# Performance work log

Measured on AMD Instinct MI355X. Metric: run time of the kernel, lower is better.

The kernel has to match this reference:

```python
import jax, jax.numpy as jnp
import numpy as np

B, S, D = 4, 2048, 1024
H = 16
HD = D // H  # 64


def setup_inputs() -> dict:
    key = jax.random.key(0)
    ks = jax.random.split(key, 6)
    s = 0.02
    return {
        "x": jax.random.normal(ks[0], (B, S, D), dtype=jnp.float32),
        "w_q": jax.random.normal(ks[1], (D, D), dtype=jnp.float32) * s,
        "w_k": jax.random.normal(ks[2], (D, D), dtype=jnp.float32) * s,
        "w_v": jax.random.normal(ks[3], (D, D), dtype=jnp.float32) * s,
        "w_o": jax.random.normal(ks[4], (D, D), dtype=jnp.float32) * s,
        "b_o": jnp.zeros((D,), dtype=jnp.float32),
    }


def reference(x, w_q, w_k, w_v, w_o, b_o):
    b, n, d_in = x.shape
    # QKV projections (torch Linear: y = x @ W^T), reshape to heads
    q = (x @ w_q.T).reshape(b, n, H, HD).transpose(0, 2, 1, 3)  # [b,h,n,hd]
    k = (x @ w_k.T).reshape(b, n, H, HD).transpose(0, 2, 1, 3)
    v = (x @ w_v.T).reshape(b, n, H, HD).transpose(0, 2, 1, 3)
    scores = jnp.einsum("bhqd,bhkd->bhqk", q, k)
    causal = jnp.triu(jnp.ones((n, n), dtype=bool), k=1)  # True above diagonal -> masked
    scores = jnp.where(causal, -jnp.inf, scores)
    attn = jax.nn.softmax(scores / jnp.sqrt(jnp.float32(HD)), axis=-1)
    # dropout p=0.0 (no-op)
    ctx = jnp.einsum("bhqk,bhkd->bhqd", attn, v)
    ctx = ctx.transpose(0, 2, 1, 3).reshape(b, n, D)
    return ctx @ w_o.T + b_o
```

## Files before the change

kernel.cpp:

```cpp
#include <hip/hip_runtime.h>
#include <hip/hip_bf16.h>

typedef __bf16 bf16x8 __attribute__((ext_vector_type(8)));
typedef float f32x4 __attribute__((ext_vector_type(4)));
typedef unsigned short u16x4 __attribute__((ext_vector_type(4)));
typedef unsigned short u16x8 __attribute__((ext_vector_type(8)));

__device__ __forceinline__ unsigned short f2bf(float f) {
  unsigned int u = __float_as_uint(f);
  u += 0x7FFFu + ((u >> 16) & 1u);
  return (unsigned short)(u >> 16);
}

__device__ __forceinline__ float exp2_fast(float x) {
  return __builtin_amdgcn_exp2f(x);
}

__device__ __forceinline__ void gld_lds16(const void* g, void* l) {
  __builtin_amdgcn_global_load_lds(
      (__attribute__((address_space(1))) void*)g,
      (__attribute__((address_space(3))) void*)l,
      16, 0, 0);
}

__global__ __launch_bounds__(256)
void cvt_bf16(const float* __restrict__ x, const float* __restrict__ wq,
              const float* __restrict__ wk, const float* __restrict__ wv,
              const float* __restrict__ wo,
              unsigned short* __restrict__ Xb, unsigned short* __restrict__ Wb)
{
  unsigned c = blockIdx.x * 256 + threadIdx.x;
  const float* src;
  unsigned short* dst;
  unsigned off;
  if (c < 1048576u) {
    src = x; dst = Xb; off = c;
  } else {
    unsigned cc = c - 1048576u;
    unsigned which = cc >> 17;
    off = cc & 131071u;
    src = which == 0 ? wq : which == 1 ? wk : which == 2 ? wv : wo;
    dst = Wb + (size_t)which * 1048576u;
  }
  f32x4 a = *reinterpret_cast<const f32x4*>(src + (size_t)off * 8);
  f32x4 b = *reinterpret_cast<const f32x4*>(src + (size_t)off * 8 + 4);
  u16x8 o = {f2bf(a.x), f2bf(a.y), f2bf(a.z), f2bf(a.w),
             f2bf(b.x), f2bf(b.y), f2bf(b.z), f2bf(b.w)};
  *reinterpret_cast<u16x8*>(dst + (size_t)off * 8) = o;
}

__global__ __launch_bounds__(256, 3)
void qkv_proj_b(const unsigned short* __restrict__ Xb, const unsigned short* __restrict__ Wb,
                unsigned short* __restrict__ Qb, unsigned short* __restrict__ Kb,
                unsigned short* __restrict__ Vb)
{
  __shared__ __align__(16) unsigned short As[128 * 64];
  __shared__ __align__(16) unsigned short Bs[128 * 64];
  char* AsB = (char*)As;
  char* BsB = (char*)Bs;

  const int z = blockIdx.z;
  const unsigned short* __restrict__ W = Wb + (size_t)z * 1048576u;
  unsigned short* __restrict__ Out = (z == 0) ? Qb : (z == 1) ? Kb : Vb;

  const int flat = blockIdx.x + (blockIdx.y << 3);
  const int swz = (flat & 7) * 64 + (flat >> 3);
  const int n0 = (swz & 7) * 128;
  const int m0 = (swz >> 3) * 128;

  const int t = threadIdx.x;
  const int lane = t & 63, wid = t >> 6;
  const int wr = wid >> 1, wc = wid & 1;
  const int l15 = lane & 15, g = lane >> 4;

  f32x4 acc[4][4] = {};

  for (int kt = 0; kt < 1024; kt += 64) {
#pragma unroll
    for (int i = 0; i < 4; ++i) {
      const int rbase = wid * 32 + i * 8;
      const int row = rbase + (lane >> 3);
      const int swzb = ((lane & 7) * 16) ^ ((row & 7) << 4);
      gld_lds16((const char*)Xb + ((size_t)(m0 + row) * 1024 + kt) * 2 + swzb,
                AsB + rbase * 128);
      gld_lds16((const char*)W + ((size_t)(n0 + row) * 1024 + kt) * 2 + swzb,
                BsB + rbase * 128);
    }
    __syncthreads();

#pragma unroll
    for (int ks = 0; ks < 2; ++ks) {
      const int kpre = ks * 64 + g * 16;
      bf16x8 af[4], bfr[4];
#pragma unroll
      for (int mi = 0; mi < 4; ++mi) {
        int row = wr * 64 + mi * 16 + l15;
        af[mi] = *reinterpret_cast<const bf16x8*>(AsB + row * 128 + (kpre ^ ((row & 7) << 4)));
      }
#pragma unroll
      for (int ni = 0; ni < 4; ++ni) {
        int row = wc * 64 + ni * 16 + l15;
        bfr[ni] = *reinterpret_cast<const bf16x8*>(BsB + row * 128 + (kpre ^ ((row & 7) << 4)));
      }
#pragma unroll
      for (int mi = 0; mi < 4; ++mi)
#pragma unroll
        for (int ni = 0; ni < 4; ++ni)
          acc[mi][ni] = __builtin_amdgcn_mfma_f32_16x16x32_bf16(af[mi], bfr[ni], acc[mi][ni], 0, 0, 0);
    }
    __syncthreads();
  }

  if (z == 2) {
#pragma unroll
    for (int mi = 0; mi < 4; ++mi)
#pragma unroll
      for (int ni = 0; ni < 4; ++ni) {
        int n = n0 + wc * 64 + ni * 16 + l15;
        int h = n >> 6, hd = n & 63;
        int m = m0 + wr * 64 + mi * 16 + 4 * g;
        int b = m >> 11, s0 = m & 2047;
        u16x4 pk = {f2bf(acc[mi][ni][0]), f2bf(acc[mi][ni][1]),
                    f2bf(acc[mi][ni][2]), f2bf(acc[mi][ni][3])};
        *reinterpret_cast<u16x4*>(Out + ((size_t)(b * 16 + h) * 64 + hd) * 2048 + s0) = pk;
      }
  } else {
    const float qs = (z == 0) ? 0.1803368801f : 1.0f;
#pragma unroll
    for (int mi = 0; mi < 4; ++mi)
#pragma unroll
      for (int ni = 0; ni < 4; ++ni)
#pragma unroll
        for (int r = 0; r < 4; ++r) {
          int m = m0 + wr * 64 + mi * 16 + 4 * g + r;
          int n = n0 + wc * 64 + ni * 16 + l15;
          int b = m >> 11, s = m & 2047;
          int h = n >> 6, hd = n & 63;
          Out[((size_t)(b * 16 + h) * 2048 + s) * 64 + hd] = f2bf(acc[mi][ni][r] * qs);
        }
  }
}

__global__ __launch_bounds__(256, 3)
void out_proj_b(const unsigned short* __restrict__ Ctx, const unsigned short* __restrict__ Wob,
                const float* __restrict__ Bo, float* __restrict__ Y)
{
  __shared__ __align__(16) unsigned short As[128 * 64];
  __shared__ __align__(16) unsigned short Bs[128 * 64];
  char* AsB = (char*)As;
  char* BsB = (char*)Bs;

  const int flat = blockIdx.x + (blockIdx.y << 3);
  const int swz = (flat & 7) * 64 + (flat >> 3);
  const int n0 = (swz & 7) * 128;
  const int m0 = (swz >> 3) * 128;

  const int t = threadIdx.x;
  const int lane = t & 63, wid = t >> 6;
  const int wr = wid >> 1, wc = wid & 1;
  const int l15 = lane & 15, g = lane >> 4;

  f32x4 acc[4][4] = {};

  for (int kt = 0; kt < 1024; kt += 64) {
#pragma unroll
    for (int i = 0; i < 4; ++i) {
      const int rbase = wid * 32 + i * 8;
      const int row = rbase + (lane >> 3);
      const int swzb = ((lane & 7) * 16) ^ ((row & 7) << 4);
      gld_lds16((const char*)Ctx + ((size_t)(m0 + row) * 1024 + kt) * 2 + swzb,
                AsB + rbase * 128);
      gld_lds16((const char*)Wob + ((size_t)(n0 + row) * 1024 + kt) * 2 + swzb,
                BsB + rbase * 128);
    }
    __syncthreads();

#pragma unroll
    for (int ks = 0; ks < 2; ++ks) {
      const int kpre = ks * 64 + g * 16;
      bf16x8 af[4], bfr[4];
#pragma unroll
      for (int mi = 0; mi < 4; ++mi) {
        int row = wr * 64 + mi * 16 + l15;
        af[mi] = *reinterpret_cast<const bf16x8*>(AsB + row * 128 + (kpre ^ ((row & 7) << 4)));
      }
#pragma unroll
      for (int ni = 0; ni < 4; ++ni) {
        int row = wc * 64 + ni * 16 + l15;
        bfr[ni] = *reinterpret_cast<const bf16x8*>(BsB + row * 128 + (kpre ^ ((row & 7) << 4)));
      }
#pragma unroll
      for (int mi = 0; mi < 4; ++mi)
#pragma unroll
        for (int ni = 0; ni < 4; ++ni)
          acc[mi][ni] = __builtin_amdgcn_mfma_f32_16x16x32_bf16(af[mi], bfr[ni], acc[mi][ni], 0, 0, 0);
    }
    __syncthreads();
  }

#pragma unroll
  for (int mi = 0; mi < 4; ++mi)
#pragma unroll
    for (int ni = 0; ni < 4; ++ni) {
      int n = n0 + wc * 64 + ni * 16 + l15;
      float bias = Bo[n];
#pragma unroll
      for (int r = 0; r < 4; ++r) {
        int m = m0 + wr * 64 + mi * 16 + 4 * g + r;
        Y[(size_t)m * 1024 + n] = acc[mi][ni][r] + bias;
      }
    }
}

__global__ __launch_bounds__(256, 2)
void attn2(const unsigned short* __restrict__ Qb, const unsigned short* __restrict__ Kb,
           const unsigned short* __restrict__ Vtg, unsigned short* __restrict__ Ctx)
{
  __shared__ __align__(16) unsigned short Ks[2][64 * 64];
  __shared__ __align__(16) unsigned short Vts[2][64 * 64];
  __shared__ __align__(16) unsigned short Pl[4][32 * 64];

  const int flat = blockIdx.x;
  const int xcd = flat & 7;
  const int idx = flat >> 3;
  const int bh = xcd * 8 + (idx >> 3);
  const int pr = idx & 7;

  const size_t base = (size_t)bh * (2048 * 64);
  const int t = threadIdx.x;
  const int lane = t & 63, wid = t >> 6;
  const int l15 = lane & 15, g = lane >> 4;
  char* PB = (char*)Pl[wid];
  const int bb = bh >> 4, hh = bh & 15;

  const int sl8 = lane >> 3;
  const int sc8 = lane & 7;
  const int pswz = (l15 & 7) << 4;

  for (int half = 0; half < 2; ++half) {
    const int tile = half ? (15 - pr) : pr;
    const int qg0 = tile * 128 + wid * 32;
    const int nst = 2 * tile + 2;

    bf16x8 qf[2][2];
#pragma unroll
    for (int mi = 0; mi < 2; ++mi)
#pragma unroll
      for (int ks = 0; ks < 2; ++ks)
        qf[mi][ks] = *reinterpret_cast<const bf16x8*>(
            Qb + base + (size_t)(qg0 + 16 * mi + l15) * 64 + ks * 32 + g * 8);

    f32x4 o[2][4] = {};
    float l_i[2] = {0.f, 0.f};

#pragma unroll
    for (int i = 0; i < 2; ++i) {
      int row = wid * 16 + i * 8 + sl8;
      int swzb = (sc8 * 16) ^ ((row & 7) << 4);
      gld_lds16((const char*)Kb + (base + (size_t)row * 64) * 2 + swzb,
                (char*)Ks[0] + (wid * 16 + i * 8) * 128);
      gld_lds16((const char*)Vtg + (base + (size_t)row * 2048) * 2 + swzb,
                (char*)Vts[0] + (wid * 16 + i * 8) * 128);
    }
    __syncthreads();

    int cur = 0;
    for (int s = 0; s < nst; ++s) {
      if (s + 1 < nst) {
#pragma unroll
        for (int i = 0; i < 2; ++i) {
          int row = wid * 16 + i * 8 + sl8;
          int swzb = (sc8 * 16) ^ ((row & 7) << 4);
          gld_lds16((const char*)Kb + (base + (size_t)((s + 1) * 64 + row) * 64) * 2 + swzb,
                    (char*)Ks[cur ^ 1] + (wid * 16 + i * 8) * 128);
          gld_lds16((const char*)Vtg + (base + (size_t)row * 2048 + (s + 1) * 64) * 2 + swzb,
                    (char*)Vts[cur ^ 1] + (wid * 16 + i * 8) * 128);
        }
      }
      char* KsB = (char*)Ks[cur];
      char* VtB = (char*)Vts[cur];

      f32x4 sw[2][4] = {};
#pragma unroll
      for (int ks = 0; ks < 2; ++ks) {
        const int kpre = ks * 64 + g * 16;
#pragma unroll
        for (int ni = 0; ni < 4; ++ni) {
          int row = ni * 16 + l15;
          bf16x8 kf = *reinterpret_cast<const bf16x8*>(KsB + row * 128 + (kpre ^ ((row & 7) << 4)));
          sw[0][ni] = __builtin_amdgcn_mfma_f32_16x16x32_bf16(kf, qf[0][ks], sw[0][ni], 0, 0, 0);
          sw[1][ni] = __builtin_amdgcn_mfma_f32_16x16x32_bf16(kf, qf[1][ks], sw[1][ni], 0, 0, 0);
        }
      }

      const bool needmask = (s * 64 + 63 > qg0);
      const int dgl = s * 64 + 4 * g - l15 - qg0;
#pragma unroll
      for (int mi = 0; mi < 2; ++mi) {
        float lsum = 0.f;
#pragma unroll
        for (int ni = 0; ni < 4; ++ni) {
          f32x4 v = sw[mi][ni];
          if (needmask) {
            int dbase = dgl + 16 * ni - 16 * mi;
#pragma unroll
            for (int r = 0; r < 4; ++r)
              if (dbase + r > 0) v[r] = -1e30f;
          }
          float p0 = exp2_fast(fminf(v[0], 60.f));
          float p1 = exp2_fast(fminf(v[1], 60.f));
          float p2 = exp2_fast(fminf(v[2], 60.f));
          float p3 = exp2_fast(fminf(v[3], 60.f));
          lsum += (p0 + p1) + (p2 + p3);
          uint2 w;
          w.x = (__float_as_uint(p0) >> 16) | (__float_as_uint(p1) & 0xFFFF0000u);
          w.y = (__float_as_uint(p2) >> 16) | (__float_as_uint(p3) & 0xFFFF0000u);
          *reinterpret_cast<uint2*>(PB + (16 * mi + l15) * 128 + ((32 * ni + 8 * g) ^ pswz)) = w;
        }
        l_i[mi] += lsum;
      }
      asm volatile("s_waitcnt lgkmcnt(0)" ::: "memory");
      __builtin_amdgcn_sched_barrier(0);

#pragma unroll
      for (int ks2 = 0; ks2 < 2; ++ks2) {
        const int kpre = ks2 * 64 + g * 16;
        bf16x8 pa0 = *reinterpret_cast<const bf16x8*>(PB + l15 * 128 + (kpre ^ pswz));
        bf16x8 pa1 = *reinterpret_cast<const bf16x8*>(PB + (16 + l15) * 128 + (kpre ^ pswz));
#pragma unroll
        for (int db = 0; db < 4; ++db) {
          int vrow = db * 16 + l15;
          bf16x8 vf = *reinterpret_cast<const bf16x8*>(VtB + vrow * 128 + (kpre ^ ((vrow & 7) << 4)));
          o[0][db] = __builtin_amdgcn_mfma_f32_16x16x32_bf16(vf, pa0, o[0][db], 0, 0, 0);
          o[1][db] = __builtin_amdgcn_mfma_f32_16x16x32_bf16(vf, pa1, o[1][db], 0, 0, 0);
        }
      }
      __syncthreads();
      cur ^= 1;
    }

#pragma unroll
    for (int mi = 0; mi < 2; ++mi) {
      float l = l_i[mi];
      l += __shfl_xor(l, 16);
      l += __shfl_xor(l, 32);
      float inv = 1.0f / l;
      int qg = qg0 + 16 * mi + l15;
#pragma unroll
      for (int db = 0; db < 4; ++db) {
        u16x4 pk = {f2bf(o[mi][db][0] * inv), f2bf(o[mi][db][1] * inv),
                    f2bf(o[mi][db][2] * inv), f2bf(o[mi][db][3] * inv)};
        *reinterpret_cast<u16x4*>(Ctx + ((size_t)(bb * 2048 + qg)) * 1024 + hh * 64 + db * 16 + 4 * g) = pk;
      }
    }
  }
}

__global__ __launch_bounds__(256, 2)
void qkv_proj(const float* __restrict__ X,
              const float* __restrict__ Wq, const float* __restrict__ Wk,
              const float* __restrict__ Wv,
              unsigned short* __restrict__ Qb, unsigned short* __restrict__ Kb,
              unsigned short* __restrict__ Vb)
{
  __shared__ __align__(16) unsigned short As[128 * 64];
  __shared__ __align__(16) unsigned short Bs[128 * 64];
  char* AsB = (char*)As;
  char* BsB = (char*)Bs;

  const float* __restrict__ W =
      (blockIdx.z == 0) ? Wq : (blockIdx.z == 1) ? Wk : Wv;
  unsigned short* __restrict__ Out =
      (blockIdx.z == 0) ? Qb : (blockIdx.z == 1) ? Kb : Vb;

  const int m0 = blockIdx.y * 128;
  const int n0 = blockIdx.x * 128;
  const int t = threadIdx.x;
  const int lane = t & 63, wid = t >> 6;
  const int wr = wid >> 1, wc = wid & 1;
  const int l15 = lane & 15, g = lane >> 4;

  f32x4 acc[4][4] = {};

  for (int kt = 0; kt < 1024; kt += 64) {
#pragma unroll
    for (int i = 0; i < 8; ++i) {
      int c = i * 256 + t;
      int row = c >> 4, c4 = c & 15;
      f32x4 a = *reinterpret_cast<const f32x4*>(X + (size_t)(m0 + row) * 1024 + kt + c4 * 4);
      f32x4 b = *reinterpret_cast<const f32x4*>(W + (size_t)(n0 + row) * 1024 + kt + c4 * 4);
      u16x4 va = {f2bf(a.x), f2bf(a.y), f2bf(a.z), f2bf(a.w)};
      u16x4 vb = {f2bf(b.x), f2bf(b.y), f2bf(b.z), f2bf(b.w)};
      int off = row * 128 + ((c4 * 8) ^ ((row & 7) << 4));
      *reinterpret_cast<u16x4*>(AsB + off) = va;
      *reinterpret_cast<u16x4*>(BsB + off) = vb;
    }
    __syncthreads();

#pragma unroll
    for (int ks = 0; ks < 2; ++ks) {
      const int kpre = ks * 64 + g * 16;
      bf16x8 af[4], bfr[4];
#pragma unroll
      for (int mi = 0; mi < 4; ++mi) {
        int row = wr * 64 + mi * 16 + l15;
        af[mi] = *reinterpret_cast<const bf16x8*>(AsB + row * 128 + (kpre ^ ((row & 7) << 4)));
      }
#pragma unroll
      for (int ni = 0; ni < 4; ++ni) {
        int row = wc * 64 + ni * 16 + l15;
        bfr[ni] = *reinterpret_cast<const bf16x8*>(BsB + row * 128 + (kpre ^ ((row & 7) << 4)));
      }
#pragma unroll
      for (int mi = 0; mi < 4; ++mi)
#pragma unroll
        for (int ni = 0; ni < 4; ++ni)
          acc[mi][ni] = __builtin_amdgcn_mfma_f32_16x16x32_bf16(af[mi], bfr[ni], acc[mi][ni], 0, 0, 0);
    }
    __syncthreads();
  }

  if (blockIdx.z == 2) {
#pragma unroll
    for (int mi = 0; mi < 4; ++mi)
#pragma unroll
      for (int ni = 0; ni < 4; ++ni) {
        int n = n0 + wc * 64 + ni * 16 + l15;
        int h = n >> 6, hd = n & 63;
        int m = m0 + wr * 64 + mi * 16 + 4 * g;
        int b = m >> 11, s0 = m & 2047;
        u16x4 pk = {f2bf(acc[mi][ni][0]), f2bf(acc[mi][ni][1]),
                    f2bf(acc[mi][ni][2]), f2bf(acc[mi][ni][3])};
        *reinterpret_cast<u16x4*>(Out + ((size_t)(b * 16 + h) * 64 + hd) * 2048 + s0) = pk;
      }
  } else {
    const float qs = (blockIdx.z == 0) ? 0.1803368801f : 1.0f;
#pragma unroll
    for (int mi = 0; mi < 4; ++mi)
#pragma unroll
      for (int ni = 0; ni < 4; ++ni)
#pragma unroll
        for (int r = 0; r < 4; ++r) {
          int m = m0 + wr * 64 + mi * 16 + 4 * g + r;
          int n = n0 + wc * 64 + ni * 16 + l15;
          int b = m >> 11, s = m & 2047;
          int h = n >> 6, hd = n & 63;
          Out[((size_t)(b * 16 + h) * 2048 + s) * 64 + hd] = f2bf(acc[mi][ni][r] * qs);
        }
  }
}

__global__ __launch_bounds__(256, 2)
void out_proj(const unsigned short* __restrict__ Ctx, const float* __restrict__ Wo,
              const float* __restrict__ Bo, float* __restrict__ Y)
{
  __shared__ __align__(16) unsigned short As[128 * 64];
  __shared__ __align__(16) unsigned short Bs[128 * 64];
  char* AsB = (char*)As;
  char* BsB = (char*)Bs;

  const int m0 = blockIdx.y * 128;
  const int n0 = blockIdx.x * 128;
  const int t = threadIdx.x;
  const int lane = t & 63, wid = t >> 6;
  const int wr = wid >> 1, wc = wid & 1;
  const int l15 = lane & 15, g = lane >> 4;

  f32x4 acc[4][4] = {};

  for (int kt = 0; kt < 1024; kt += 64) {
#pragma unroll
    for (int i = 0; i < 4; ++i) {
      int c = i * 256 + t;
      int row = c >> 3, c8 = c & 7;
      bf16x8 v = *reinterpret_cast<const bf16x8*>(Ctx + (size_t)(m0 + row) * 1024 + kt + c8 * 8);
      *reinterpret_cast<bf16x8*>(AsB + row * 128 + ((c8 * 16) ^ ((row & 7) << 4))) = v;
    }
#pragma unroll
    for (int i = 0; i < 8; ++i) {
      int c = i * 256 + t;
      int row = c >> 4, c4 = c & 15;
      f32x4 b = *reinterpret_cast<const f32x4*>(Wo + (size_t)(n0 + row) * 1024 + kt + c4 * 4);
      u16x4 vb = {f2bf(b.x), f2bf(b.y), f2bf(b.z), f2bf(b.w)};
      *reinterpret_cast<u16x4*>(BsB + row * 128 + ((c4 * 8) ^ ((row & 7) << 4))) = vb;
    }
    __syncthreads();

#pragma unroll
    for (int ks = 0; ks < 2; ++ks) {
      const int kpre = ks * 64 + g * 16;
      bf16x8 af[4], bfr[4];
#pragma unroll
      for (int mi = 0; mi < 4; ++mi) {
        int row = wr * 64 + mi * 16 + l15;
        af[mi] = *reinterpret_cast<const bf16x8*>(AsB + row * 128 + (kpre ^ ((row & 7) << 4)));
      }
#pragma unroll
      for (int ni = 0; ni < 4; ++ni) {
        int row = wc * 64 + ni * 16 + l15;
        bfr[ni] = *reinterpret_cast<const bf16x8*>(BsB + row * 128 + (kpre ^ ((row & 7) << 4)));
      }
#pragma unroll
      for (int mi = 0; mi < 4; ++mi)
#pragma unroll
        for (int ni = 0; ni < 4; ++ni)
          acc[mi][ni] = __builtin_amdgcn_mfma_f32_16x16x32_bf16(af[mi], bfr[ni], acc[mi][ni], 0, 0, 0);
    }
    __syncthreads();
  }

#pragma unroll
  for (int mi = 0; mi < 4; ++mi)
#pragma unroll
    for (int ni = 0; ni < 4; ++ni) {
      int n = n0 + wc * 64 + ni * 16 + l15;
      float bias = Bo[n];
#pragma unroll
      for (int r = 0; r < 4; ++r) {
        int m = m0 + wr * 64 + mi * 16 + 4 * g + r;
        Y[(size_t)m * 1024 + n] = acc[mi][ni][r] + bias;
      }
    }
}

__global__ __launch_bounds__(256, 4)
void attn(const unsigned short* __restrict__ Qb, const unsigned short* __restrict__ Kb,
          const unsigned short* __restrict__ Vtg, unsigned short* __restrict__ Ctx)
{
  __shared__ __align__(16) unsigned short Ks[2][64 * 64];
  __shared__ __align__(16) unsigned short Vts[2][64 * 64];
  __shared__ __align__(16) unsigned short Pl[4][16 * 64];

  const int flat = blockIdx.x;
  const int xcd = flat & 7;
  const int idx = flat >> 3;
  const int bh = xcd * 8 + (idx >> 4);
  const int p = idx & 15;

  const size_t base = (size_t)bh * (2048 * 64);
  const int t = threadIdx.x;
  const int lane = t & 63, wid = t >> 6;
  const int l15 = lane & 15, g = lane >> 4;
  char* PB = (char*)Pl[wid];

  const int srow = t >> 3;
  const int sc8 = t & 7;

  const int bb = bh >> 4, hh = bh & 15;

  for (int half = 0; half < 2; ++half) {
    const int qt = half ? (31 - p) : p;
    const int q0 = qt * 64 + wid * 16;

    bf16x8 qf[2];
#pragma unroll
    for (int ks = 0; ks < 2; ++ks)
      qf[ks] = *reinterpret_cast<const bf16x8*>(Qb + base + (size_t)(q0 + l15) * 64 + ks * 32 + g * 8);

    f32x4 o[4] = {};
    float m_i[4] = {-INFINITY, -INFINITY, -INFINITY, -INFINITY};
    float l_i[4] = {0.f, 0.f, 0.f, 0.f};

    bf16x8 kreg[2], vreg[2];
#pragma unroll
    for (int i = 0; i < 2; ++i) {
      int row = srow + i * 32;
      kreg[i] = *reinterpret_cast<const bf16x8*>(Kb + base + (size_t)row * 64 + sc8 * 8);
      vreg[i] = *reinterpret_cast<const bf16x8*>(Vtg + base + (size_t)row * 2048 + sc8 * 8);
    }
#pragma unroll
    for (int i = 0; i < 2; ++i) {
      int row = srow + i * 32;
      int off = row * 128 + ((sc8 * 16) ^ ((row & 7) << 4));
      *reinterpret_cast<bf16x8*>((char*)Ks[0] + off) = kreg[i];
      *reinterpret_cast<bf16x8*>((char*)Vts[0] + off) = vreg[i];
    }
    __syncthreads();

    int cur = 0;
    for (int s = 0; s <= qt; ++s) {
      if (s < qt) {
#pragma unroll
        for (int i = 0; i < 2; ++i) {
          int row = srow + i * 32;
          kreg[i] = *reinterpret_cast<const bf16x8*>(Kb + base + (size_t)((s + 1) * 64 + row) * 64 + sc8 * 8);
          vreg[i] = *reinterpret_cast<const bf16x8*>(Vtg + base + (size_t)row * 2048 + (s + 1) * 64 + sc8 * 8);
        }
      }
      char* KsB = (char*)Ks[cur];
      char* VtB = (char*)Vts[cur];

      f32x4 sc[4] = {};
#pragma unroll
      for (int ks = 0; ks < 2; ++ks) {
        const int kpre = ks * 64 + g * 16;
#pragma unroll
        for (int ni = 0; ni < 4; ++ni) {
          int row = ni * 16 + l15;
          bf16x8 kf = *reinterpret_cast<const bf16x8*>(KsB + row * 128 + (kpre ^ ((row & 7) << 4)));
          sc[ni] = __builtin_amdgcn_mfma_f32_16x16x32_bf16(qf[ks], kf, sc[ni], 0, 0, 0);
        }
      }

      if (s == qt) {
#pragma unroll
        for (int ni = 0; ni < 4; ++ni)
#pragma unroll
          for (int r = 0; r < 4; ++r)
            if ((ni * 16 + l15) > (wid * 16 + 4 * g + r)) sc[ni][r] = -1e30f;
      }

      float alpha[4];
#pragma unroll
      for (int r = 0; r < 4; ++r) {
        float mx = fmaxf(fmaxf(sc[0][r], sc[1][r]), fmaxf(sc[2][r], sc[3][r]));
#pragma unroll
        for (int off = 8; off >= 1; off >>= 1)
          mx = fmaxf(mx, __shfl_xor(mx, off, 16));
        float mnew = fmaxf(m_i[r], mx);
        alpha[r] = exp2_fast(m_i[r] - mnew);
        m_i[r] = mnew;
        float ps = 0.f;
#pragma unroll
        for (int ni = 0; ni < 4; ++ni) {
          float pp = exp2_fast(sc[ni][r] - mnew);
          sc[ni][r] = pp;
          ps += pp;
        }
        l_i[r] = l_i[r] * alpha[r] + ps;
      }

#pragma unroll
      for (int db = 0; db < 4; ++db)
#pragma unroll
        for (int r = 0; r < 4; ++r)
          o[db][r] *= alpha[r];

#pragma unroll
      for (int ni = 0; ni < 4; ++ni)
#pragma unroll
        for (int r = 0; r < 4; ++r) {
          int ii = 4 * g + r, j = ni * 16 + l15;
          *reinterpret_cast<unsigned short*>(PB + ii * 128 + ((j * 2) ^ ((ii & 7) << 4))) =
              (unsigned short)(__float_as_uint(sc[ni][r]) >> 16);
        }

#pragma unroll
      for (int ks2 = 0; ks2 < 2; ++ks2) {
        const int kpre = ks2 * 64 + g * 16;
        bf16x8 pa = *reinterpret_cast<const bf16x8*>(PB + l15 * 128 + (kpre ^ ((l15 & 7) << 4)));
#pragma unroll
        for (int db = 0; db < 4; ++db) {
          int vrow = db * 16 + l15;
          bf16x8 vf = *reinterpret_cast<const bf16x8*>(VtB + vrow * 128 + (kpre ^ ((vrow & 7) << 4)));
          o[db] = __builtin_amdgcn_mfma_f32_16x16x32_bf16(pa, vf, o[db], 0, 0, 0);
        }
      }

      if (s < qt) {
#pragma unroll
        for (int i = 0; i < 2; ++i) {
          int row = srow + i * 32;
          int off = row * 128 + ((sc8 * 16) ^ ((row & 7) << 4));
          *reinterpret_cast<bf16x8*>((char*)Ks[cur ^ 1] + off) = kreg[i];
          *reinterpret_cast<bf16x8*>((char*)Vts[cur ^ 1] + off) = vreg[i];
        }
      }
      __syncthreads();
      cur ^= 1;
    }

#pragma unroll
    for (int r = 0; r < 4; ++r) {
      float l = l_i[r];
#pragma unroll
      for (int off = 8; off >= 1; off >>= 1)
        l += __shfl_xor(l, off, 16);
      l_i[r] = 1.0f / l;
    }
#pragma unroll
    for (int db = 0; db < 4; ++db)
#pragma unroll
      for (int r = 0; r < 4; ++r) {
        int q = q0 + 4 * g + r;
        float val = o[db][r] * l_i[r];
        Ctx[((size_t)(bb * 2048 + q)) * 1024 + hh * 64 + db * 16 + l15] = f2bf(val);
      }
  }
}

extern "C" void kernel_launch(void* const* d_in, const int* in_sizes, int n_in,
                              void* d_out, int out_size, void* d_ws, size_t ws_size,
                              hipStream_t stream)
{
  const float* x  = (const float*)d_in[0];
  const float* wq = (const float*)d_in[1];
  const float* wk = (const float*)d_in[2];
  const float* wv = (const float*)d_in[3];
  const float* wo = (const float*)d_in[4];
  const float* bo = (const float*)d_in[5];
  float* y = (float*)d_out;

  if (ws_size >= 75497472ULL) {
    unsigned short* Xb = (unsigned short*)d_ws;
    unsigned short* Qb = Xb + 8388608;
    unsigned short* Kb = Qb + 8388608;
    unsigned short* Vb = Kb + 8388608;
    unsigned short* Wb = Vb + 8388608;
    unsigned short* Cx = Xb;

    cvt_bf16<<<6144, 256, 0, stream>>>(x, wq, wk, wv, wo, Xb, Wb);
    qkv_proj_b<<<dim3(8, 64, 3), 256, 0, stream>>>(Xb, Wb, Qb, Kb, Vb);
    attn2<<<512, 256, 0, stream>>>(Qb, Kb, Vb, Cx);
    out_proj_b<<<dim3(8, 64), 256, 0, stream>>>(Cx, Wb + 3 * 1048576, bo, y);
  } else {
    unsigned short* Qb = (unsigned short*)d_ws;
    unsigned short* Kb = Qb + 8388608;
    unsigned short* Vb = Kb + 8388608;
    unsigned short* Cx = Vb + 8388608;

    qkv_proj<<<dim3(8, 64, 3), 256, 0, stream>>>(x, wq, wk, wv, Qb, Kb, Vb);
    attn<<<1024, 256, 0, stream>>>(Qb, Kb, Vb, Cx);
    out_proj<<<dim3(8, 64), 256, 0, stream>>>(Cx, wo, bo, y);
  }
}
```

Baseline: 161.4 us.

## Split causal attention KV range across two kernels with partial-sum merge

Adds an attention kernel that splits each 128-row query tile's causal KV range into two halves run as separate launches. The first launch writes unnormalized bf16 partial outputs and row sums to workspace, and the second adds its half, normalizes and writes context. The aim is to balance per-block work and raise parallelism over the single attn2 launch. It only runs when the workspace is large enough, which is unknown. It adds an extra launch and a bf16 round-trip of the partials, drops the exp2 clamp (overflow risk with no running max), and the fallback path now calls attn2 in place of attn.

```diff
diff --git a/kernel.cpp b/kernel.cpp
--- a/kernel.cpp
+++ b/kernel.cpp
@@ -10,6 +10,10 @@
   unsigned int u = __float_as_uint(f);
   u += 0x7FFFu + ((u >> 16) & 1u);
   return (unsigned short)(u >> 16);
+}
+
+__device__ __forceinline__ float bf2f(unsigned short b) {
+  return __uint_as_float((unsigned)b << 16);
 }
 
 __device__ __forceinline__ float exp2_fast(float x) {
@@ -212,6 +216,166 @@
     }
 }
 
+template<bool FIRST>
+__global__ __launch_bounds__(256, 3)
+void attn_split(const unsigned short* __restrict__ Qb, const unsigned short* __restrict__ Kb,
+                const unsigned short* __restrict__ Vtg,
+                unsigned short* __restrict__ Part, float* __restrict__ Lp,
+                unsigned short* __restrict__ Ctx)
+{
+  __shared__ __align__(16) unsigned short Ks[2][64 * 64];
+  __shared__ __align__(16) unsigned short Vts[2][64 * 64];
+  __shared__ __align__(16) unsigned short Pl[4][32 * 64];
+
+  const int flat = blockIdx.x;
+  const int xcd = flat & 7;
+  const int j = flat >> 3;
+  const int tile = 15 - (j >> 3);
+  const int bh = xcd * 8 + (j & 7);
+
+  const size_t base = (size_t)bh * (2048 * 64);
+  const int t = threadIdx.x;
+  const int lane = t & 63, wid = t >> 6;
+  const int l15 = lane & 15, g = lane >> 4;
+  char* PB = (char*)Pl[wid];
+  const int bb = bh >> 4, hh = bh & 15;
+
+  const int sl8 = lane >> 3;
+  const int sc8 = lane & 7;
+  const int pswz = (l15 & 7) << 4;
+
+  const int qg0 = tile * 128 + wid * 32;
+  const int s0   = FIRST ? 0 : (tile + 1);
+  const int send = FIRST ? (tile + 1) : (2 * tile + 2);
+
+  bf16x8 qf[2][2];
+#pragma unroll
+  for (int mi = 0; mi < 2; ++mi)
+#pragma unroll
+    for (int ks = 0; ks < 2; ++ks)
+      qf[mi][ks] = *reinterpret_cast<const bf16x8*>(
+          Qb + base + (size_t)(qg0 + 16 * mi + l15) * 64 + ks * 32 + g * 8);
+
+  f32x4 o[2][4] = {};
+  float l_i[2] = {0.f, 0.f};
+
+#pragma unroll
+  for (int i = 0; i < 2; ++i) {
+    int row = wid * 16 + i * 8 + sl8;
+    int swzb = (sc8 * 16) ^ ((row & 7) << 4);
+    gld_lds16((const char*)Kb + (base + (size_t)(s0 * 64 + row) * 64) * 2 + swzb,
+              (char*)Ks[0] + (wid * 16 + i * 8) * 128);
+    gld_lds16((const char*)Vtg + (base + (size_t)row * 2048 + s0 * 64) * 2 + swzb,
+              (char*)Vts[0] + (wid * 16 + i * 8) * 128);
+  }
+  __syncthreads();
+
+  int cur = 0;
+  for (int s = s0; s < send; ++s) {
+    if (s + 1 < send) {
+#pragma unroll
+      for (int i = 0; i < 2; ++i) {
+        int row = wid * 16 + i * 8 + sl8;
+        int swzb = (sc8 * 16) ^ ((row & 7) << 4);
+        gld_lds16((const char*)Kb + (base + (size_t)((s + 1) * 64 + row) * 64) * 2 + swzb,
+                  (char*)Ks[cur ^ 1] + (wid * 16 + i * 8) * 128);
+        gld_lds16((const char*)Vtg + (base + (size_t)row * 2048 + (s + 1) * 64) * 2 + swzb,
+                  (char*)Vts[cur ^ 1] + (wid * 16 + i * 8) * 128);
+      }
+    }
+    char* KsB = (char*)Ks[cur];
+    char* VtB = (char*)Vts[cur];
+
+    f32x4 sw[2][4] = {};
+#pragma unroll
+    for (int ks = 0; ks < 2; ++ks) {
+      const int kpre = ks * 64 + g * 16;
+#pragma unroll
+      for (int ni = 0; ni < 4; ++ni) {
+        int row = ni * 16 + l15;
+        bf16x8 kf = *reinterpret_cast<const bf16x8*>(KsB + row * 128 + (kpre ^ ((row & 7) << 4)));
+        sw[0][ni] = __builtin_amdgcn_mfma_f32_16x16x32_bf16(kf, qf[0][ks], sw[0][ni], 0, 0, 0);
+        sw[1][ni] = __builtin_amdgcn_mfma_f32_16x16x32_bf16(kf, qf[1][ks], sw[1][ni], 0, 0, 0);
+      }
+    }
+
+    const bool needmask = (s * 64 + 63 > qg0);
+    const int dgl = s * 64 + 4 * g - l15 - qg0;
+#pragma unroll
+    for (int mi = 0; mi < 2; ++mi) {
+      float lsum = 0.f;
+#pragma unroll
+      for (int ni = 0; ni < 4; ++ni) {
+        f32x4 v = sw[mi][ni];
+        if (needmask) {
+          int dbase = dgl + 16 * ni - 16 * mi;
+#pragma unroll
+          for (int r = 0; r < 4; ++r)
+            if (dbase + r > 0) v[r] = -1e30f;
+        }
+        float p0 = exp2_fast(v[0]);
+        float p1 = exp2_fast(v[1]);
+        float p2 = exp2_fast(v[2]);
+        float p3 = exp2_fast(v[3]);
+        lsum += (p0 + p1) + (p2 + p3);
+        uint2 w;
+        w.x = (__float_as_uint(p0) >> 16) | (__float_as_uint(p1) & 0xFFFF0000u);
+        w.y = (__float_as_uint(p2) >> 16) | (__float_as_uint(p3) & 0xFFFF0000u);
+        *reinterpret_cast<uint2*>(PB + (16 * mi + l15) * 128 + ((32 * ni + 8 * g) ^ pswz)) = w;
+      }
+      l_i[mi] += lsum;
+    }
+    asm volatile("s_waitcnt lgkmcnt(0)" ::: "memory");
+    __builtin_amdgcn_sched_barrier(0);
+
+#pragma unroll
+    for (int ks2 = 0; ks2 < 2; ++ks2) {
+      const int kpre = ks2 * 64 + g * 16;
+      bf16x8 pa0 = *reinterpret_cast<const bf16x8*>(PB + l15 * 128 + (kpre ^ pswz));
+      bf16x8 pa1 = *reinterpret_cast<const bf16x8*>(PB + (16 + l15) * 128 + (kpre ^ pswz));
+#pragma unroll
+      for (int db = 0; db < 4; ++db) {
+        int vrow = db * 16 + l15;
+        bf16x8 vf = *reinterpret_cast<const bf16x8*>(VtB + vrow * 128 + (kpre ^ ((vrow & 7) << 4)));
+        o[0][db] = __builtin_amdgcn_mfma_f32_16x16x32_bf16(vf, pa0, o[0][db], 0, 0, 0);
+        o[1][db] = __builtin_amdgcn_mfma_f32_16x16x32_bf16(vf, pa1, o[1][db], 0, 0, 0);
+      }
+    }
+    __syncthreads();
+    cur ^= 1;
+  }
+
+#pragma unroll
+  for (int mi = 0; mi < 2; ++mi) {
+    float l = l_i[mi];
+    l += __shfl_xor(l, 16);
+    l += __shfl_xor(l, 32);
+    int qg = qg0 + 16 * mi + l15;
+    size_t pidx = ((size_t)bh * 2048 + qg) * 64;
+    if (FIRST) {
+      if (g == 0) Lp[(size_t)bh * 2048 + qg] = l;
+#pragma unroll
+      for (int db = 0; db < 4; ++db) {
+        u16x4 pk = {f2bf(o[mi][db][0]), f2bf(o[mi][db][1]),
+                    f2bf(o[mi][db][2]), f2bf(o[mi][db][3])};
+        *reinterpret_cast<u16x4*>(Part + pidx + db * 16 + 4 * g) = pk;
+      }
+    } else {
+      float lt = l + Lp[(size_t)bh * 2048 + qg];
+      float inv = 1.0f / lt;
+#pragma unroll
+      for (int db = 0; db < 4; ++db) {
+        u16x4 pp = *reinterpret_cast<const u16x4*>(Part + pidx + db * 16 + 4 * g);
+        u16x4 pk = {f2bf((o[mi][db][0] + bf2f(pp[0])) * inv),
+                    f2bf((o[mi][db][1] + bf2f(pp[1])) * inv),
+                    f2bf((o[mi][db][2] + bf2f(pp[2])) * inv),
+                    f2bf((o[mi][db][3] + bf2f(pp[3])) * inv)};
+        *reinterpret_cast<u16x4*>(Ctx + ((size_t)(bb * 2048 + qg)) * 1024 + hh * 64 + db * 16 + 4 * g) = pk;
+      }
+    }
+  }
+}
+
 __global__ __launch_bounds__(256, 2)
 void attn2(const unsigned short* __restrict__ Qb, const unsigned short* __restrict__ Kb,
            const unsigned short* __restrict__ Vtg, unsigned short* __restrict__ Ctx)
@@ -307,10 +471,10 @@
             for (int r = 0; r < 4; ++r)
               if (dbase + r > 0) v[r] = -1e30f;
           }
-          float p0 = exp2_fast(fminf(v[0], 60.f));
-          float p1 = exp2_fast(fminf(v[1], 60.f));
-          float p2 = exp2_fast(fminf(v[2], 60.f));
-          float p3 = exp2_fast(fminf(v[3], 60.f));
+          float p0 = exp2_fast(v[0]);
+          float p1 = exp2_fast(v[1]);
+          float p2 = exp2_fast(v[2]);
+          float p3 = exp2_fast(v[3]);
           lsum += (p0 + p1) + (p2 + p3);
           uint2 w;
           w.x = (__float_as_uint(p0) >> 16) | (__float_as_uint(p1) & 0xFFFF0000u);
@@ -523,172 +687,6 @@
     }
 }
 
-__global__ __launch_bounds__(256, 4)
-void attn(const unsigned short* __restrict__ Qb, const unsigned short* __restrict__ Kb,
-          const unsigned short* __restrict__ Vtg, unsigned short* __restrict__ Ctx)
-{
-  __shared__ __align__(16) unsigned short Ks[2][64 * 64];
-  __shared__ __align__(16) unsigned short Vts[2][64 * 64];
-  __shared__ __align__(16) unsigned short Pl[4][16 * 64];
-
-  const int flat = blockIdx.x;
-  const int xcd = flat & 7;
-  const int idx = flat >> 3;
-  const int bh = xcd * 8 + (idx >> 4);
-  const int p = idx & 15;
-
-  const size_t base = (size_t)bh * (2048 * 64);
-  const int t = threadIdx.x;
-  const int lane = t & 63, wid = t >> 6;
-  const int l15 = lane & 15, g = lane >> 4;
-  char* PB = (char*)Pl[wid];
-
-  const int srow = t >> 3;
-  const int sc8 = t & 7;
-
-  const int bb = bh >> 4, hh = bh & 15;
-
-  for (int half = 0; half < 2; ++half) {
-    const int qt = half ? (31 - p) : p;
-    const int q0 = qt * 64 + wid * 16;
-
-    bf16x8 qf[2];
-#pragma unroll
-    for (int ks = 0; ks < 2; ++ks)
-      qf[ks] = *reinterpret_cast<const bf16x8*>(Qb + base + (size_t)(q0 + l15) * 64 + ks * 32 + g * 8);
-
-    f32x4 o[4] = {};
-    float m_i[4] = {-INFINITY, -INFINITY, -INFINITY, -INFINITY};
-    float l_i[4] = {0.f, 0.f, 0.f, 0.f};
-
-    bf16x8 kreg[2], vreg[2];
-#pragma unroll
-    for (int i = 0; i < 2; ++i) {
-      int row = srow + i * 32;
-      kreg[i] = *reinterpret_cast<const bf16x8*>(Kb + base + (size_t)row * 64 + sc8 * 8);
-      vreg[i] = *reinterpret_cast<const bf16x8*>(Vtg + base + (size_t)row * 2048 + sc8 * 8);
-    }
-#pragma unroll
-    for (int i = 0; i < 2; ++i) {
-      int row = srow + i * 32;
-      int off = row * 128 + ((sc8 * 16) ^ ((row & 7) << 4));
-      *reinterpret_cast<bf16x8*>((char*)Ks[0] + off) = kreg[i];
-      *reinterpret_cast<bf16x8*>((char*)Vts[0] + off) = vreg[i];
-    }
-    __syncthreads();
-
-    int cur = 0;
-    for (int s = 0; s <= qt; ++s) {
-      if (s < qt) {
-#pragma unroll
-        for (int i = 0; i < 2; ++i) {
-          int row = srow + i * 32;
-          kreg[i] = *reinterpret_cast<const bf16x8*>(Kb + base + (size_t)((s + 1) * 64 + row) * 64 + sc8 * 8);
-          vreg[i] = *reinterpret_cast<const bf16x8*>(Vtg + base + (size_t)row * 2048 + (s + 1) * 64 + sc8 * 8);
-        }
-      }
-      char* KsB = (char*)Ks[cur];
-      char* VtB = (char*)Vts[cur];
-
-      f32x4 sc[4] = {};
-#pragma unroll
-      for (int ks = 0; ks < 2; ++ks) {
-        const int kpre = ks * 64 + g * 16;
-#pragma unroll
-        for (int ni = 0; ni < 4; ++ni) {
-          int row = ni * 16 + l15;
-          bf16x8 kf = *reinterpret_cast<const bf16x8*>(KsB + row * 128 + (kpre ^ ((row & 7) << 4)));
-          sc[ni] = __builtin_amdgcn_mfma_f32_16x16x32_bf16(qf[ks], kf, sc[ni], 0, 0, 0);
-        }
-      }
-
-      if (s == qt) {
-#pragma unroll
-        for (int ni = 0; ni < 4; ++ni)
-#pragma unroll
-          for (int r = 0; r < 4; ++r)
-            if ((ni * 16 + l15) > (wid * 16 + 4 * g + r)) sc[ni][r] = -1e30f;
-      }
-
-      float alpha[4];
-#pragma unroll
-      for (int r = 0; r < 4; ++r) {
-        float mx = fmaxf(fmaxf(sc[0][r], sc[1][r]), fmaxf(sc[2][r], sc[3][r]));
-#pragma unroll
-        for (int off = 8; off >= 1; off >>= 1)
-          mx = fmaxf(mx, __shfl_xor(mx, off, 16));
-        float mnew = fmaxf(m_i[r], mx);
-        alpha[r] = exp2_fast(m_i[r] - mnew);
-        m_i[r] = mnew;
-        float ps = 0.f;
-#pragma unroll
-        for (int ni = 0; ni < 4; ++ni) {
-          float pp = exp2_fast(sc[ni][r] - mnew);
-          sc[ni][r] = pp;
-          ps += pp;
-        }
-        l_i[r] = l_i[r] * alpha[r] + ps;
-      }
-
-#pragma unroll
-      for (int db = 0; db < 4; ++db)
-#pragma unroll
-        for (int r = 0; r < 4; ++r)
-          o[db][r] *= alpha[r];
-
-#pragma unroll
-      for (int ni = 0; ni < 4; ++ni)
-#pragma unroll
-        for (int r = 0; r < 4; ++r) {
-          int ii = 4 * g + r, j = ni * 16 + l15;
-          *reinterpret_cast<unsigned short*>(PB + ii * 128 + ((j * 2) ^ ((ii & 7) << 4))) =
-              (unsigned short)(__float_as_uint(sc[ni][r]) >> 16);
-        }
-
-#pragma unroll
-      for (int ks2 = 0; ks2 < 2; ++ks2) {
-        const int kpre = ks2 * 64 + g * 16;
-        bf16x8 pa = *reinterpret_cast<const bf16x8*>(PB + l15 * 128 + (kpre ^ ((l15 & 7) << 4)));
-#pragma unroll
-        for (int db = 0; db < 4; ++db) {
-          int vrow = db * 16 + l15;
-          bf16x8 vf = *reinterpret_cast<const bf16x8*>(VtB + vrow * 128 + (kpre ^ ((vrow & 7) << 4)));
-          o[db] = __builtin_amdgcn_mfma_f32_16x16x32_bf16(pa, vf, o[db], 0, 0, 0);
-        }
-      }
-
-      if (s < qt) {
-#pragma unroll
-        for (int i = 0; i < 2; ++i) {
-          int row = srow + i * 32;
-          int off = row * 128 + ((sc8 * 16) ^ ((row & 7) << 4));
-          *reinterpret_cast<bf16x8*>((char*)Ks[cur ^ 1] + off) = kreg[i];
-          *reinterpret_cast<bf16x8*>((char*)Vts[cur ^ 1] + off) = vreg[i];
-        }
-      }
-      __syncthreads();
-      cur ^= 1;
-    }
-
-#pragma unroll
-    for (int r = 0; r < 4; ++r) {
-      float l = l_i[r];
-#pragma unroll
-      for (int off = 8; off >= 1; off >>= 1)
-        l += __shfl_xor(l, off, 16);
-      l_i[r] = 1.0f / l;
-    }
-#pragma unroll
-    for (int db = 0; db < 4; ++db)
-#pragma unroll
-      for (int r = 0; r < 4; ++r) {
-        int q = q0 + 4 * g + r;
-        float val = o[db][r] * l_i[r];
-        Ctx[((size_t)(bb * 2048 + q)) * 1024 + hh * 64 + db * 16 + l15] = f2bf(val);
-      }
-  }
-}
-
 extern "C" void kernel_launch(void* const* d_in, const int* in_sizes, int n_in,
                               void* d_out, int out_size, void* d_ws, size_t ws_size,
                               hipStream_t stream)
@@ -711,7 +709,16 @@
 
     cvt_bf16<<<6144, 256, 0, stream>>>(x, wq, wk, wv, wo, Xb, Wb);
     qkv_proj_b<<<dim3(8, 64, 3), 256, 0, stream>>>(Xb, Wb, Qb, Kb, Vb);
-    attn2<<<512, 256, 0, stream>>>(Qb, Kb, Vb, Cx);
+
+    if (ws_size >= 92798976ULL) {
+      unsigned short* Part = Wb + 4194304;
+      float* Lp = (float*)(Part + 8388608);
+      attn_split<true><<<1024, 256, 0, stream>>>(Qb, Kb, Vb, Part, Lp, Cx);
+      attn_split<false><<<1024, 256, 0, stream>>>(Qb, Kb, Vb, Part, Lp, Cx);
+    } else {
+      attn2<<<512, 256, 0, stream>>>(Qb, Kb, Vb, Cx);
+    }
+
     out_proj_b<<<dim3(8, 64), 256, 0, stream>>>(Cx, Wb + 3 * 1048576, bo, y);
   } else {
     unsigned short* Qb = (unsigned short*)d_ws;
@@ -720,7 +727,7 @@
     unsigned short* Cx = Vb + 8388608;
 
     qkv_proj<<<dim3(8, 64, 3), 256, 0, stream>>>(x, wq, wk, wv, Qb, Kb, Vb);
-    attn<<<1024, 256, 0, stream>>>(Qb, Kb, Vb, Cx);
+    attn2<<<512, 256, 0, stream>>>(Qb, Kb, Vb, Cx);
     out_proj<<<dim3(8, 64), 256, 0, stream>>>(Cx, wo, bo, y);
   }
 }
```

New measurement: 161.2 us. No clear change (-0.1%).
